# Kernel optimization log

Hardware: AMD Instinct MI355X
Metric: run time of the kernel (lower is better)

## Reference

```python
import jax, jax.numpy as jnp
import numpy as np

NEG_SLOPE = 0.2


def setup_inputs() -> dict:
    key = jax.random.key(0)
    k_h, k_adj, k_dis, k_w, k_we, k_a = jax.random.split(key, 6)
    B, N, D, H = 16, 200, 128, 8
    n = D // H  # per-head hidden = 16
    h = jax.random.normal(k_h, (B, N, D), dtype=jnp.float32)
    adj_mat = jax.random.randint(k_adj, (B, N, N, 1), 0, 2, dtype=jnp.int32)
    dis_mat = jax.random.normal(k_dis, (B, N, N, D), dtype=jnp.float32)
    scale = 1.0 / np.sqrt(D)
    W = jax.random.normal(k_w, (D, D), dtype=jnp.float32) * scale      # self.linear.weight.T
    W_e = jax.random.normal(k_we, (D, D), dtype=jnp.float32) * scale   # self.linear_e.weight.T
    a = jax.random.normal(k_a, (3 * n,), dtype=jnp.float32) * (1.0 / np.sqrt(3 * n))  # self.attn.weight
    return {"h": h, "adj_mat": adj_mat, "dis_mat": dis_mat, "W": W, "W_e": W_e, "a": a}


def reference(h, adj_mat, dis_mat, W, W_e, a):
    B, N, D = h.shape
    n = a.shape[0] // 3          # per-head hidden
    H = D // n                   # nb_heads
    g = (h @ W).reshape(B, N, H, n)                 # [B,N,H,n]
    E = (dis_mat @ W_e).reshape(B, N, N, H, n)      # [B,N,N,H,n]
    # attn(cat([g_i, g_j, E_ij])) == g_i@a1 + g_j@a2 + E_ij@a3
    a1, a2, a3 = a[:n], a[n:2 * n], a[2 * n:]
    s_i = jnp.einsum('bihn,n->bih', g, a1)          # varies over row i (repeat_interleave)
    s_j = jnp.einsum('bjhn,n->bjh', g, a2)          # varies over col j (repeat)
    s_e = jnp.einsum('bijhn,n->bijh', E, a3)
    e = jax.nn.leaky_relu(s_i[:, :, None, :] + s_j[:, None, :, :] + s_e, NEG_SLOPE)
    e = jnp.where(adj_mat == 0, -jnp.inf, e)        # adj [B,N,N,1] broadcasts over heads
    attn = jax.nn.softmax(e, axis=2)                # softmax over j
    out = jnp.einsum('bijh,bjhf->bihf', attn, g)
    return out.reshape(B, N, H * n)
```

## Files before the change

### kernel.cpp

```cpp
#include <hip/hip_runtime.h>
#include <math.h>

constexpr int B = 16, N = 200, D = 128, H = 8;
constexpr int JT = 40;
constexpr float NEG_SLOPE = 0.2f;

__global__ void prep_v(const float* __restrict__ We, const float* __restrict__ a,
                       float* __restrict__ v) {
    int d = threadIdx.x;
    float a3[16];
#pragma unroll
    for (int nn = 0; nn < 16; ++nn) a3[nn] = a[32 + nn];
    for (int h = 0; h < H; ++h) {
        float s = 0.f;
#pragma unroll
        for (int nn = 0; nn < 16; ++nn) s = fmaf(We[d * D + h * 16 + nn], a3[nn], s);
        v[h * D + d] = s;
    }
}

__global__ void prep_g(const float* __restrict__ hmat, const float* __restrict__ W,
                       const float* __restrict__ a,
                       float* __restrict__ g, float* __restrict__ s_i,
                       float* __restrict__ s_j) {
    const int row = blockIdx.x;
    const int t = threadIdx.x;
    __shared__ __align__(16) float hrow[D];
    __shared__ float p1[D], p2[D];
    if (t < 32) ((float4*)hrow)[t] = ((const float4*)(hmat + (size_t)row * D))[t];
    __syncthreads();
    float acc = 0.f;
#pragma unroll 4
    for (int d = 0; d < D; ++d) acc = fmaf(hrow[d], W[d * D + t], acc);
    g[(size_t)row * D + t] = acc;
    p1[t] = acc * a[t & 15];
    p2[t] = acc * a[16 + (t & 15)];
    __syncthreads();
    if (t < H) {
        float s1 = 0.f, s2 = 0.f;
#pragma unroll
        for (int nn = 0; nn < 16; ++nn) { s1 += p1[t * 16 + nn]; s2 += p2[t * 16 + nn]; }
        s_i[row * H + t] = s1;
        s_j[row * H + t] = s2;
    }
}

__global__ void __launch_bounds__(320)
attn_fused(const float* __restrict__ dis, const int* __restrict__ adj,
           const float* __restrict__ g, const float* __restrict__ s_i,
           const float* __restrict__ s_j, const float* __restrict__ v,
           float* __restrict__ out) {
    const int bi = blockIdx.x;
    const int b  = bi / N;
    const int t  = threadIdx.x;

    __shared__ __align__(16) float ds_tile[JT][132];
    __shared__ __align__(16) float se[N][H];
    __shared__ __align__(16) float sjs[N][H];
    __shared__ __align__(16) float vv[H][132];
    __shared__ int   adjs[N];
    __shared__ float red[256];
    __shared__ float sis[H], maxh[H], invh[H];

    if (t < 256) {
        float4 x = ((const float4*)v)[t];
        int hh = t >> 5, dd = (t & 31) * 4;
        vv[hh][dd] = x.x; vv[hh][dd + 1] = x.y; vv[hh][dd + 2] = x.z; vv[hh][dd + 3] = x.w;
    }
    {
        const float4* sj4 = (const float4*)(s_j + (size_t)b * N * H);
        float4* dst = (float4*)&sjs[0][0];
        for (int f = t; f < 400; f += 320) dst[f] = sj4[f];
    }
    if (t < N) adjs[t] = adj[(size_t)bi * N + t];
    if (t < H) sis[t] = s_i[(size_t)bi * H + t];
    __syncthreads();

    for (int tile = 0; tile < N / JT; ++tile) {
        const int j0 = tile * JT;
        const float4* src = (const float4*)(dis + ((size_t)bi * N + j0) * D);
        for (int f = t; f < JT * D / 4; f += 320) {
            float4 x = src[f];
            int r = f >> 5, c = (f & 31) * 4;
            *(float4*)&ds_tile[r][c] = x;
        }
        __syncthreads();
        {
            const int j = t >> 3, h = t & 7;
            float s = 0.f;
#pragma unroll
            for (int d = 0; d < D; d += 4) {
                float4 x = *(const float4*)&ds_tile[j][d];
                float4 w = *(const float4*)&vv[h][d];
                s = fmaf(x.x, w.x, s); s = fmaf(x.y, w.y, s);
                s = fmaf(x.z, w.z, s); s = fmaf(x.w, w.w, s);
            }
            se[j0 + j][h] = s;
        }
        __syncthreads();
    }

    for (int idx = t; idx < N * H; idx += 320) {
        int j = idx >> 3, h = idx & 7;
        float val = sis[h] + sjs[j][h] + se[j][h];
        val = val > 0.f ? val : NEG_SLOPE * val;
        se[j][h] = (adjs[j] != 0) ? val : -__builtin_inff();
    }
    __syncthreads();

    {
        const int h = t & 7, jr = t >> 3;
        float m = -__builtin_inff();
        for (int j = jr; j < N; j += 40) m = fmaxf(m, se[j][h]);
        m = fmaxf(m, __shfl_xor(m, 8));
        m = fmaxf(m, __shfl_xor(m, 16));
        m = fmaxf(m, __shfl_xor(m, 32));
        if ((t & 63) < 8) red[(t >> 6) * 8 + h] = m;
    }
    __syncthreads();
    if (t < 8) {
        float m = red[t];
        for (int w = 1; w < 5; ++w) m = fmaxf(m, red[w * 8 + t]);
        maxh[t] = m;
    }
    __syncthreads();
    {
        const int h = t & 7, jr = t >> 3;
        const float mh = maxh[h];
        float s = 0.f;
        for (int j = jr; j < N; j += 40) {
            float x = se[j][h];
            float p = (x == -__builtin_inff()) ? 0.f : __expf(x - mh);
            se[j][h] = p;
            s += p;
        }
        s += __shfl_xor(s, 8);
        s += __shfl_xor(s, 16);
        s += __shfl_xor(s, 32);
        if ((t & 63) < 8) red[(t >> 6) * 8 + h] = s;
    }
    __syncthreads();
    if (t < 8) {
        float s = red[t];
        for (int w = 1; w < 5; ++w) s += red[w * 8 + t];
        invh[t] = (s > 0.f) ? 1.f / s : 0.f;
    }
    __syncthreads();

    if (t < 256) {
        const int hf = t & 127, jpar = t >> 7;
        const float* gb = g + (size_t)b * N * D + hf;
        float acc = 0.f;
#pragma unroll 4
        for (int j = jpar; j < N; j += 2)
            acc = fmaf(se[j][hf >> 4], gb[(size_t)j * D], acc);
        red[t] = acc;
    }
    __syncthreads();
    if (t < 128)
        out[(size_t)bi * D + t] = (red[t] + red[t + 128]) * invh[t >> 4];
}

extern "C" void kernel_launch(void* const* d_in, const int* in_sizes, int n_in,
                              void* d_out, int out_size, void* d_ws, size_t ws_size,
                              hipStream_t stream) {
    const float* hmat = (const float*)d_in[0];
    const int*   adj  = (const int*)d_in[1];
    const float* dis  = (const float*)d_in[2];
    const float* W    = (const float*)d_in[3];
    const float* We   = (const float*)d_in[4];
    const float* a    = (const float*)d_in[5];
    float* out = (float*)d_out;

    float* ws  = (float*)d_ws;
    float* v   = ws;
    float* g   = ws + 1024;
    float* s_i = g + (size_t)B * N * D;
    float* s_j = s_i + (size_t)B * N * H;

    prep_v<<<1, 128, 0, stream>>>(We, a, v);
    prep_g<<<B * N, 128, 0, stream>>>(hmat, W, a, g, s_i, s_j);
    attn_fused<<<B * N, 320, 0, stream>>>(dis, adj, g, s_i, s_j, v, out);
}
```

Baseline: 520.0 us.

## Stream dis rows directly into registers with DPP reductions and merge prep kernels

Replaces the LDS-staged dis tiles in the attention kernel with per-wave register streaming. Each group of 16 lanes loads one 128-float row with a one-step prefetch, dots it against v held in registers for all heads, and reduces across lanes with DPP row shifts. This removes the tile barriers and shared-memory round trips. It also merges the two prep kernels into one launch, splits the g accumulation into four chains, fuses the leaky-relu/mask pass into the max pass, and adds an occupancy hint, at the cost of higher register pressure from the v and prefetch registers.

```diff
diff --git a/kernel.cpp b/kernel.cpp
--- a/kernel.cpp
+++ b/kernel.cpp
@@ -2,36 +2,49 @@
 #include <math.h>
 
 constexpr int B = 16, N = 200, D = 128, H = 8;
-constexpr int JT = 40;
 constexpr float NEG_SLOPE = 0.2f;
 
-__global__ void prep_v(const float* __restrict__ We, const float* __restrict__ a,
-                       float* __restrict__ v) {
-    int d = threadIdx.x;
-    float a3[16];
-#pragma unroll
-    for (int nn = 0; nn < 16; ++nn) a3[nn] = a[32 + nn];
-    for (int h = 0; h < H; ++h) {
-        float s = 0.f;
-#pragma unroll
-        for (int nn = 0; nn < 16; ++nn) s = fmaf(We[d * D + h * 16 + nn], a3[nn], s);
-        v[h * D + d] = s;
-    }
-}
-
-__global__ void prep_g(const float* __restrict__ hmat, const float* __restrict__ W,
-                       const float* __restrict__ a,
-                       float* __restrict__ g, float* __restrict__ s_i,
-                       float* __restrict__ s_j) {
+template<int CTRL>
+__device__ __forceinline__ float dpp_add(float x) {
+    union { float f; int i; } u, r;
+    u.f = x;
+    r.i = __builtin_amdgcn_update_dpp(0, u.i, CTRL, 0xf, 0xf, true);
+    return x + r.f;
+}
+
+__global__ void prep_all(const float* __restrict__ hmat, const float* __restrict__ W,
+                         const float* __restrict__ We, const float* __restrict__ a,
+                         float* __restrict__ g, float* __restrict__ s_i,
+                         float* __restrict__ s_j, float* __restrict__ v) {
     const int row = blockIdx.x;
     const int t = threadIdx.x;
+
+    if (row == B * N) {
+        float a3[16];
+#pragma unroll
+        for (int nn = 0; nn < 16; ++nn) a3[nn] = a[32 + nn];
+        for (int h = 0; h < H; ++h) {
+            float s = 0.f;
+#pragma unroll
+            for (int nn = 0; nn < 16; ++nn) s = fmaf(We[t * D + h * 16 + nn], a3[nn], s);
+            v[h * D + t] = s;
+        }
+        return;
+    }
+
     __shared__ __align__(16) float hrow[D];
     __shared__ float p1[D], p2[D];
     if (t < 32) ((float4*)hrow)[t] = ((const float4*)(hmat + (size_t)row * D))[t];
     __syncthreads();
-    float acc = 0.f;
-#pragma unroll 4
-    for (int d = 0; d < D; ++d) acc = fmaf(hrow[d], W[d * D + t], acc);
+    float c0 = 0.f, c1 = 0.f, c2 = 0.f, c3 = 0.f;
+#pragma unroll 8
+    for (int d = 0; d < D; d += 4) {
+        c0 = fmaf(hrow[d],     W[(d)     * D + t], c0);
+        c1 = fmaf(hrow[d + 1], W[(d + 1) * D + t], c1);
+        c2 = fmaf(hrow[d + 2], W[(d + 2) * D + t], c2);
+        c3 = fmaf(hrow[d + 3], W[(d + 3) * D + t], c3);
+    }
+    float acc = (c0 + c1) + (c2 + c3);
     g[(size_t)row * D + t] = acc;
     p1[t] = acc * a[t & 15];
     p2[t] = acc * a[16 + (t & 15)];
@@ -45,7 +58,7 @@
     }
 }
 
-__global__ void __launch_bounds__(320)
+__global__ void __launch_bounds__(320, 4)
 attn_fused(const float* __restrict__ dis, const int* __restrict__ adj,
            const float* __restrict__ g, const float* __restrict__ s_i,
            const float* __restrict__ s_j, const float* __restrict__ v,
@@ -53,69 +66,85 @@
     const int bi = blockIdx.x;
     const int b  = bi / N;
     const int t  = threadIdx.x;
-
-    __shared__ __align__(16) float ds_tile[JT][132];
+    const int wave = t >> 6;
+    const int lane = t & 63;
+    const int grp  = lane >> 4;
+    const int c    = lane & 15;
+
     __shared__ __align__(16) float se[N][H];
     __shared__ __align__(16) float sjs[N][H];
-    __shared__ __align__(16) float vv[H][132];
     __shared__ int   adjs[N];
     __shared__ float red[256];
     __shared__ float sis[H], maxh[H], invh[H];
 
-    if (t < 256) {
-        float4 x = ((const float4*)v)[t];
-        int hh = t >> 5, dd = (t & 31) * 4;
-        vv[hh][dd] = x.x; vv[hh][dd + 1] = x.y; vv[hh][dd + 2] = x.z; vv[hh][dd + 3] = x.w;
-    }
+    float4 va[H], vb[H];
+#pragma unroll
+    for (int h = 0; h < H; ++h) {
+        va[h] = *(const float4*)(v + h * D + 4 * c);
+        vb[h] = *(const float4*)(v + h * D + 64 + 4 * c);
+    }
+
     {
         const float4* sj4 = (const float4*)(s_j + (size_t)b * N * H);
         float4* dst = (float4*)&sjs[0][0];
-        for (int f = t; f < 400; f += 320) dst[f] = sj4[f];
+        for (int f = t; f < N * H / 4; f += 320) dst[f] = sj4[f];
     }
     if (t < N) adjs[t] = adj[(size_t)bi * N + t];
     if (t < H) sis[t] = s_i[(size_t)bi * H + t];
-    __syncthreads();
-
-    for (int tile = 0; tile < N / JT; ++tile) {
-        const int j0 = tile * JT;
-        const float4* src = (const float4*)(dis + ((size_t)bi * N + j0) * D);
-        for (int f = t; f < JT * D / 4; f += 320) {
-            float4 x = src[f];
-            int r = f >> 5, c = (f & 31) * 4;
-            *(float4*)&ds_tile[r][c] = x;
-        }
-        __syncthreads();
-        {
-            const int j = t >> 3, h = t & 7;
-            float s = 0.f;
-#pragma unroll
-            for (int d = 0; d < D; d += 4) {
-                float4 x = *(const float4*)&ds_tile[j][d];
-                float4 w = *(const float4*)&vv[h][d];
-                s = fmaf(x.x, w.x, s); s = fmaf(x.y, w.y, s);
-                s = fmaf(x.z, w.z, s); s = fmaf(x.w, w.w, s);
-            }
-            se[j0 + j][h] = s;
-        }
-        __syncthreads();
-    }
-
-    for (int idx = t; idx < N * H; idx += 320) {
-        int j = idx >> 3, h = idx & 7;
-        float val = sis[h] + sjs[j][h] + se[j][h];
-        val = val > 0.f ? val : NEG_SLOPE * val;
-        se[j][h] = (adjs[j] != 0) ? val : -__builtin_inff();
-    }
-    __syncthreads();
-
+
+    const float* dbase = dis + ((size_t)bi * N + wave * 40 + grp) * D + 4 * c;
+    float4 cA = *(const float4*)(dbase);
+    float4 cB = *(const float4*)(dbase + 64);
+#pragma unroll 2
+    for (int it = 0; it < 10; ++it) {
+        float4 nA, nB;
+        if (it < 9) {
+            nA = *(const float4*)(dbase + (it + 1) * 4 * D);
+            nB = *(const float4*)(dbase + (it + 1) * 4 * D + 64);
+        }
+        float acc[H];
+#pragma unroll
+        for (int h = 0; h < H; ++h) {
+            acc[h] = fmaf(cA.x, va[h].x, fmaf(cA.y, va[h].y,
+                     fmaf(cA.z, va[h].z, fmaf(cA.w, va[h].w,
+                     fmaf(cB.x, vb[h].x, fmaf(cB.y, vb[h].y,
+                     fmaf(cB.z, vb[h].z, cB.w * vb[h].w)))))));
+        }
+#pragma unroll
+        for (int h = 0; h < H; ++h) {
+            float x = acc[h];
+            x = dpp_add<0x121>(x);
+            x = dpp_add<0x122>(x);
+            x = dpp_add<0x124>(x);
+            x = dpp_add<0x128>(x);
+            acc[h] = x;
+        }
+        if (c == 0) {
+            const int row = wave * 40 + it * 4 + grp;
+            *(float4*)&se[row][0] = float4{acc[0], acc[1], acc[2], acc[3]};
+            *(float4*)&se[row][4] = float4{acc[4], acc[5], acc[6], acc[7]};
+        }
+        cA = nA; cB = nB;
+    }
+    __syncthreads();
+
+    const int h8 = t & 7, jr = t >> 3;
     {
-        const int h = t & 7, jr = t >> 3;
+        const float si = sis[h8];
         float m = -__builtin_inff();
-        for (int j = jr; j < N; j += 40) m = fmaxf(m, se[j][h]);
+#pragma unroll
+        for (int k = 0; k < 5; ++k) {
+            const int j = jr + 40 * k;
+            float val = si + sjs[j][h8] + se[j][h8];
+            val = val > 0.f ? val : NEG_SLOPE * val;
+            val = adjs[j] ? val : -__builtin_inff();
+            se[j][h8] = val;
+            m = fmaxf(m, val);
+        }
         m = fmaxf(m, __shfl_xor(m, 8));
         m = fmaxf(m, __shfl_xor(m, 16));
         m = fmaxf(m, __shfl_xor(m, 32));
-        if ((t & 63) < 8) red[(t >> 6) * 8 + h] = m;
+        if (lane < 8) red[wave * 8 + h8] = m;
     }
     __syncthreads();
     if (t < 8) {
@@ -125,19 +154,20 @@
     }
     __syncthreads();
     {
-        const int h = t & 7, jr = t >> 3;
-        const float mh = maxh[h];
+        const float mh = maxh[h8];
         float s = 0.f;
-        for (int j = jr; j < N; j += 40) {
-            float x = se[j][h];
-            float p = (x == -__builtin_inff()) ? 0.f : __expf(x - mh);
-            se[j][h] = p;
+#pragma unroll
+        for (int k = 0; k < 5; ++k) {
+            const int j = jr + 40 * k;
+            const float x = se[j][h8];
+            const float p = (x == -__builtin_inff()) ? 0.f : __expf(x - mh);
+            se[j][h8] = p;
             s += p;
         }
         s += __shfl_xor(s, 8);
         s += __shfl_xor(s, 16);
         s += __shfl_xor(s, 32);
-        if ((t & 63) < 8) red[(t >> 6) * 8 + h] = s;
+        if (lane < 8) red[wave * 8 + h8] = s;
     }
     __syncthreads();
     if (t < 8) {
@@ -178,7 +208,6 @@
     float* s_i = g + (size_t)B * N * D;
     float* s_j = s_i + (size_t)B * N * H;
 
-    prep_v<<<1, 128, 0, stream>>>(We, a, v);
-    prep_g<<<B * N, 128, 0, stream>>>(hmat, W, a, g, s_i, s_j);
+    prep_all<<<B * N + 1, 128, 0, stream>>>(hmat, W, We, a, g, s_i, s_j, v);
     attn_fused<<<B * N, 320, 0, stream>>>(dis, adj, g, s_i, s_j, v, out);
 }
```

New measurement: 482.9 us. 1.08x faster.
